# Performance work log

Measured on AMD Instinct MI355X. Metric: run time of the kernel, lower is better.

The kernel has to match this reference:

```python
import jax, jax.numpy as jnp
import numpy as np

EMBED_DIM = 512
SE_HIDDEN = max(1, int(EMBED_DIM * 0.25))  # 128
LN_EPS = 1e-5


def setup_inputs() -> dict:
    key = jax.random.key(0)
    ks = jax.random.split(key, 16)
    B, H, W, D = 8, 32, 32, EMBED_DIM
    s = 0.02
    return {
        "q": jax.random.normal(ks[0], (B, H, W, D), jnp.float32),
        "k": jax.random.normal(ks[1], (B, H, W, D), jnp.float32),
        "v": jax.random.normal(ks[2], (B, H, W, D), jnp.float32),
        # Linear weights stored as [in, out] (equivalent to torch W.T)
        "Wq": jax.random.normal(ks[3], (D, D), jnp.float32) * s,
        "Wk": jax.random.normal(ks[4], (D, D), jnp.float32) * s,
        "Wv": jax.random.normal(ks[5], (D, D), jnp.float32) * s,
        "Wo": jax.random.normal(ks[6], (D, D), jnp.float32) * s,
        # Conv2d kernel in HWIO layout for NHWC conv
        "conv_w": jax.random.normal(ks[7], (3, 3, D, D), jnp.float32) * s,
        "conv_b": jnp.zeros((D,), jnp.float32),
        "se_w1": jax.random.normal(ks[8], (D, SE_HIDDEN), jnp.float32) * s,
        "se_b1": jnp.zeros((SE_HIDDEN,), jnp.float32),
        "se_w2": jax.random.normal(ks[9], (SE_HIDDEN, D), jnp.float32) * s,
        "se_b2": jnp.zeros((D,), jnp.float32),
        "ln_g": jnp.ones((D,), jnp.float32),
        "ln_b": jnp.zeros((D,), jnp.float32),
    }


def _layernorm(x, g, b):
    mu = jnp.mean(x, axis=-1, keepdims=True)
    var = jnp.mean(jnp.square(x - mu), axis=-1, keepdims=True)
    return (x - mu) * jax.lax.rsqrt(var + LN_EPS) * g + b


def reference(q, k, v, Wq, Wk, Wv, Wo, conv_w, conv_b,
              se_w1, se_b1, se_w2, se_b2, ln_g, ln_b):
    B, H, W, D = q.shape
    scaler = jnp.sqrt(jnp.asarray(D, q.dtype))
    qp = q @ Wq  # [B,H,W,D]
    kp = k @ Wk
    vp = v @ Wv
    N = H * W
    qf = qp.reshape(B, N, D)
    kf = kp.reshape(B, N, D)
    vf = vp.reshape(B, N, D)
    scores = jnp.einsum('bnd,bmd->bnm', qf, kf) / scaler
    probs = jax.nn.softmax(scores, axis=-1)  # dropout p=0 -> identity
    out = jnp.einsum('bnm,bmd->bnd', probs, vf).reshape(B, H, W, D)
    out = out @ Wo
    # 3x3 same conv in NHWC
    out = jax.lax.conv_general_dilated(
        out, conv_w, window_strides=(1, 1), padding='SAME',
        dimension_numbers=('NHWC', 'HWIO', 'NHWC')) + conv_b
    # squeeze-excite: global average pool over spatial dims
    se = jnp.mean(out, axis=(1, 2))  # [B,D]
    se = jax.nn.silu(se @ se_w1 + se_b1)
    se = jax.nn.sigmoid(se @ se_w2 + se_b2)  # [B,D]
    out = out * se[:, None, None, :]
    x = qp + out  # residual uses q AFTER q_proj (q reassigned in torch code)
    return _layernorm(x, ln_g, ln_b)
```

## Files before the change

### kernel.cpp

```cpp
#include <hip/hip_runtime.h>
#include <hip/hip_bf16.h>

using bf16 = __hip_bfloat16;
typedef __attribute__((ext_vector_type(8))) short short8;
typedef __attribute__((ext_vector_type(4))) short short4v;
typedef __attribute__((ext_vector_type(4))) float f32x4;

static const size_t OFF_QP   = 0;
static const size_t OFF_KP   = (size_t)8  << 20;
static const size_t OFF_VPT  = (size_t)16 << 20;
static const size_t OFF_SC   = (size_t)24 << 20;
static const size_t OFF_WT   = (size_t)56 << 20;
static const size_t OFF_CWT  = (size_t)58 << 20;
static const size_t OFF_POOL = (size_t)63 << 20;
static const size_t OFF_SE   = ((size_t)63 << 20) + 16384;

__global__ __launch_bounds__(256) void prep_k(const float* __restrict__ Wq,
                                              const float* __restrict__ Wk,
                                              const float* __restrict__ Wv,
                                              const float* __restrict__ Wo,
                                              const float* __restrict__ convw,
                                              bf16* __restrict__ wT,
                                              bf16* __restrict__ cwT,
                                              float* __restrict__ pooled) {
    long idx = (long)blockIdx.x * 256 + threadIdx.x;
    if (idx < 4l * 262144) {
        int m = (int)(idx >> 18);
        int o = (int)(idx & 262143);
        int n = o >> 9, k = o & 511;
        const float* W = (m == 0) ? Wq : (m == 1) ? Wk : (m == 2) ? Wv : Wo;
        wT[idx] = __float2bfloat16(W[k * 512 + n]);
    } else if (idx < 4l * 262144 + 512l * 4608) {
        long o = idx - 4l * 262144;
        int co = (int)(o / 4608), t = (int)(o % 4608);
        cwT[o] = __float2bfloat16(convw[(long)t * 512 + co]);
    } else if (idx < 4l * 262144 + 512l * 4608 + 4096) {
        pooled[idx - (4l * 262144 + 512l * 4608)] = 0.f;
    }
}

template <int OP>
__global__ __launch_bounds__(256, 2) void gemm_k(
    const void* __restrict__ Ap0, const void* __restrict__ Ap1, const void* __restrict__ Ap2,
    int lda, long sA,
    const bf16* __restrict__ BT, int ldb, long sB,
    void* __restrict__ Cp, int ldc, long sC,
    int K, const float* __restrict__ bias, float* __restrict__ pooled) {
    __shared__ bf16 As[2][128 * 64];
    __shared__ bf16 Bs[2][128 * 64];
    const int tid = threadIdx.x;
    const int l = tid & 63, w = tid >> 6;
    const int wm = w >> 1, wn = w & 1;

    const int gx = gridDim.x, gy = gridDim.y;
    const int nwg = gx * gy * gridDim.z;
    const int bid = blockIdx.x + gx * (blockIdx.y + gy * blockIdx.z);
    const int swz = (bid & 7) * (nwg >> 3) + (bid >> 3);
    const int bx = swz % gx;
    const int rem = swz / gx;
    const int by = rem % gy;
    const int zb = rem / gy;

    const int m0 = by * 128, n0 = bx * 128;
    const float isc = 0.04419417382415922f;

    const bf16* Ab = nullptr;
    const float* Af = nullptr;
    if (OP == 1) {
        Af = (const float*)(zb == 0 ? Ap0 : zb == 1 ? Ap1 : Ap2);
    } else {
        Ab = (const bf16*)Ap0 + (long)zb * sA;
    }
    const bf16* Bb = BT + (OP == 1 ? (long)zb * 262144 : (long)zb * sB);

    const int fr = l & 15;
    f32x4 acc[4][4] = {};

    int pixoff[4], hh_[4], wp_[4];
    if (OP == 3) {
#pragma unroll
        for (int i = 0; i < 4; ++i) {
            int s = tid + i * 256;
            int row = s >> 3, c = s & 7;
            int p = m0 + row;
            int bb = p >> 10;
            hh_[i] = (p >> 5) & 31;
            wp_[i] = p & 31;
            pixoff[i] = ((bb * 32 + hh_[i]) * 32 + wp_[i]) * 512 + c * 8;
        }
    }

    short8 ar[4];
    float4 af0[4], af1[4];
    short8 br[4];

    auto stage_load = [&](int t) {
        int k0 = t * 64;
        int dy = 0, dx = 0, doff = 0;
        if (OP == 3) {
            int tap = k0 >> 9;
            dy = tap / 3 - 1;
            dx = tap % 3 - 1;
            doff = (dy * 32 + dx) * 512 + (k0 & 511);
        }
#pragma unroll
        for (int i = 0; i < 4; ++i) {
            int s = tid + i * 256;
            int row = s >> 3, c = s & 7;
            if (OP == 1) {
                const float* src = Af + (long)(m0 + row) * lda + k0 + c * 8;
                af0[i] = *(const float4*)src;
                af1[i] = *(const float4*)(src + 4);
            } else if (OP == 3) {
                int h2 = hh_[i] + dy, w2 = wp_[i] + dx;
                if (((unsigned)h2 < 32u) & ((unsigned)w2 < 32u)) {
                    ar[i] = *(const short8*)(Ab + pixoff[i] + doff);
                } else {
                    short8 zz = {0, 0, 0, 0, 0, 0, 0, 0};
                    ar[i] = zz;
                }
            } else {
                ar[i] = *(const short8*)(Ab + (long)(m0 + row) * lda + k0 + c * 8);
            }
        }
#pragma unroll
        for (int i = 0; i < 4; ++i) {
            int s = tid + i * 256;
            int row = s >> 3, c = s & 7;
            br[i] = *(const short8*)(Bb + (long)(n0 + row) * ldb + k0 + c * 8);
        }
    };

    auto stage_write = [&](int b) {
#pragma unroll
        for (int i = 0; i < 4; ++i) {
            int s = tid + i * 256;
            int row = s >> 3, c = s & 7;
            int cx = c ^ (row & 7);
            if (OP == 1) {
                union { short8 s8; bf16 h[8]; } u;
                u.h[0] = __float2bfloat16(af0[i].x); u.h[1] = __float2bfloat16(af0[i].y);
                u.h[2] = __float2bfloat16(af0[i].z); u.h[3] = __float2bfloat16(af0[i].w);
                u.h[4] = __float2bfloat16(af1[i].x); u.h[5] = __float2bfloat16(af1[i].y);
                u.h[6] = __float2bfloat16(af1[i].z); u.h[7] = __float2bfloat16(af1[i].w);
                *(short8*)(&As[b][row * 64 + cx * 8]) = u.s8;
            } else {
                *(short8*)(&As[b][row * 64 + cx * 8]) = ar[i];
            }
        }
#pragma unroll
        for (int i = 0; i < 4; ++i) {
            int s = tid + i * 256;
            int row = s >> 3, c = s & 7;
            int cx = c ^ (row & 7);
            *(short8*)(&Bs[b][row * 64 + cx * 8]) = br[i];
        }
    };

    auto compute = [&](int b) {
#pragma unroll
        for (int h = 0; h < 2; ++h) {
            int cx = ((l >> 4) + 4 * h) ^ (fr & 7);
            short8 afr[4], bfv[4];
#pragma unroll
            for (int m = 0; m < 4; ++m) {
                int r = wm * 64 + m * 16 + fr;
                afr[m] = *(const short8*)(&As[b][r * 64 + cx * 8]);
            }
#pragma unroll
            for (int n = 0; n < 4; ++n) {
                int r = wn * 64 + n * 16 + fr;
                bfv[n] = *(const short8*)(&Bs[b][r * 64 + cx * 8]);
            }
#pragma unroll
            for (int m = 0; m < 4; ++m)
#pragma unroll
                for (int n = 0; n < 4; ++n)
                    acc[m][n] = __builtin_amdgcn_mfma_f32_16x16x32_bf16(afr[m], bfv[n], acc[m][n], 0, 0, 0);
        }
    };

    const int nt = K >> 6;
    stage_load(0);
    stage_write(0);
    int cur = 0;
    for (int t = 0; t < nt; ++t) {
        __syncthreads();
        if (t + 1 < nt) stage_load(t + 1);
        compute(cur);
        if (t + 1 < nt) stage_write(cur ^ 1);
        cur ^= 1;
    }

    const int cr = (l >> 4) * 4, cc = l & 15;
    float csum[4] = {0.f, 0.f, 0.f, 0.f};
#pragma unroll
    for (int m = 0; m < 4; ++m) {
#pragma unroll
        for (int n = 0; n < 4; ++n) {
#pragma unroll
            for (int j = 0; j < 4; ++j) {
                int r = m0 + wm * 64 + m * 16 + cr + j;
                int c = n0 + wn * 64 + n * 16 + cc;
                float vv = acc[m][n][j];
                if (OP == 3) {
                    vv += bias[c];
                    csum[n] += vv;
                    ((bf16*)Cp)[(long)r * ldc + c] = __float2bfloat16(vv);
                } else if (OP == 0 || OP == 2) {
                    ((bf16*)Cp)[(long)zb * sC + (long)r * ldc + c] = __float2bfloat16(vv);
                } else {
                    if (zb == 2) {
                        ((bf16*)Cp)[(size_t)(OFF_VPT / 2) + ((long)(r >> 10) * 512 + c) * 1024 + (r & 1023)] =
                            __float2bfloat16(vv);
                    } else {
                        float sv = (zb == 1) ? vv * isc : vv;
                        ((bf16*)Cp)[(long)zb * 4194304 + (long)r * 512 + c] = __float2bfloat16(sv);
                    }
                }
            }
        }
    }
    if (OP == 3) {
        int bb = m0 >> 10;
#pragma unroll
        for (int n = 0; n < 4; ++n) {
            int c = n0 + wn * 64 + n * 16 + cc;
            atomicAdd(&pooled[bb * 512 + c], csum[n] * (1.0f / 1024.0f));
        }
    }
}

__global__ __launch_bounds__(256) void softmax_k(bf16* __restrict__ scores) {
    __shared__ float red[256];
    long row = blockIdx.x;
    bf16* base = scores + row * 1024;
    int t = threadIdx.x;
    union { short4v s4; bf16 h[4]; } u;
    u.s4 = *(const short4v*)(base + t * 4);
    float v[4];
#pragma unroll
    for (int i = 0; i < 4; ++i) v[i] = __bfloat162float(u.h[i]);
    float mx = fmaxf(fmaxf(v[0], v[1]), fmaxf(v[2], v[3]));
    red[t] = mx;
    __syncthreads();
    for (int s = 128; s > 0; s >>= 1) {
        if (t < s) red[t] = fmaxf(red[t], red[t + s]);
        __syncthreads();
    }
    mx = red[0];
    __syncthreads();
    float e[4], sum = 0.f;
#pragma unroll
    for (int i = 0; i < 4; ++i) {
        e[i] = __expf(v[i] - mx);
        sum += e[i];
    }
    red[t] = sum;
    __syncthreads();
    for (int s = 128; s > 0; s >>= 1) {
        if (t < s) red[t] += red[t + s];
        __syncthreads();
    }
    float inv = 1.0f / red[0];
#pragma unroll
    for (int i = 0; i < 4; ++i) u.h[i] = __float2bfloat16(e[i] * inv);
    *(short4v*)(base + t * 4) = u.s4;
}

__global__ __launch_bounds__(512) void se_mlp_k(const float* __restrict__ pooled,
                                                const float* __restrict__ w1,
                                                const float* __restrict__ b1,
                                                const float* __restrict__ w2,
                                                const float* __restrict__ b2,
                                                float* __restrict__ se) {
    __shared__ float pl[512];
    __shared__ float part[4][128];
    __shared__ float hid[128];
    const int b = blockIdx.x, t = threadIdx.x;
    pl[t] = pooled[b * 512 + t];
    __syncthreads();
    const int j = t & 127, r = t >> 7;
    float acc = 0.f;
#pragma unroll 8
    for (int s = 0; s < 128; ++s) {
        int i = r * 128 + s;
        acc += pl[i] * w1[i * 128 + j];
    }
    part[r][j] = acc;
    __syncthreads();
    if (t < 128) {
        float a = part[0][t] + part[1][t] + part[2][t] + part[3][t] + b1[t];
        hid[t] = a / (1.f + __expf(-a));
    }
    __syncthreads();
    float acc2 = b2[t];
#pragma unroll 8
    for (int jj = 0; jj < 128; ++jj)
        acc2 += hid[jj] * w2[jj * 512 + t];
    se[b * 512 + t] = 1.f / (1.f + __expf(-acc2));
}

__global__ __launch_bounds__(256) void final_k(const bf16* __restrict__ conv_out,
                                               const float* __restrict__ se,
                                               const bf16* __restrict__ qp,
                                               const float* __restrict__ g,
                                               const float* __restrict__ bta,
                                               float* __restrict__ out) {
    __shared__ float red[256];
    long p = blockIdx.x;
    int b = (int)(p >> 10);
    int t = threadIdx.x;
    float x[2];
#pragma unroll
    for (int i = 0; i < 2; ++i) {
        int c = t + i * 256;
        x[i] = __bfloat162float(qp[p * 512 + c]) +
               __bfloat162float(conv_out[p * 512 + c]) * se[b * 512 + c];
    }
    red[t] = x[0] + x[1];
    __syncthreads();
    for (int s = 128; s > 0; s >>= 1) {
        if (t < s) red[t] += red[t + s];
        __syncthreads();
    }
    float mu = red[0] * (1.0f / 512.0f);
    __syncthreads();
    float d0 = x[0] - mu, d1 = x[1] - mu;
    red[t] = d0 * d0 + d1 * d1;
    __syncthreads();
    for (int s = 128; s > 0; s >>= 1) {
        if (t < s) red[t] += red[t + s];
        __syncthreads();
    }
    float inv = rsqrtf(red[0] * (1.0f / 512.0f) + 1e-5f);
#pragma unroll
    for (int i = 0; i < 2; ++i) {
        int c = t + i * 256;
        out[p * 512 + c] = (x[i] - mu) * inv * g[c] + bta[c];
    }
}

extern "C" void kernel_launch(void* const* d_in, const int* in_sizes, int n_in,
                              void* d_out, int out_size, void* d_ws, size_t ws_size,
                              hipStream_t stream) {
    const float* q      = (const float*)d_in[0];
    const float* k      = (const float*)d_in[1];
    const float* v      = (const float*)d_in[2];
    const float* Wq     = (const float*)d_in[3];
    const float* Wk     = (const float*)d_in[4];
    const float* Wv     = (const float*)d_in[5];
    const float* Wo     = (const float*)d_in[6];
    const float* convw  = (const float*)d_in[7];
    const float* convb  = (const float*)d_in[8];
    const float* se_w1  = (const float*)d_in[9];
    const float* se_b1  = (const float*)d_in[10];
    const float* se_w2  = (const float*)d_in[11];
    const float* se_b2  = (const float*)d_in[12];
    const float* ln_g   = (const float*)d_in[13];
    const float* ln_b   = (const float*)d_in[14];

    char* ws = (char*)d_ws;
    bf16*  qp     = (bf16*)(ws + OFF_QP);
    bf16*  kp     = (bf16*)(ws + OFF_KP);
    bf16*  attn   = (bf16*)(ws + OFF_KP);
    bf16*  vpT    = (bf16*)(ws + OFF_VPT);
    bf16*  out2   = (bf16*)(ws + OFF_VPT);
    bf16*  scores = (bf16*)(ws + OFF_SC);
    bf16*  convo  = (bf16*)(ws + OFF_SC);
    bf16*  wT     = (bf16*)(ws + OFF_WT);
    bf16*  cwT    = (bf16*)(ws + OFF_CWT);
    float* pooled = (float*)(ws + OFF_POOL);
    float* se     = (float*)(ws + OFF_SE);

    prep_k<<<13328, 256, 0, stream>>>(Wq, Wk, Wv, Wo, convw, wT, cwT, pooled);

    gemm_k<1><<<dim3(4, 64, 3), 256, 0, stream>>>(q, k, v, 512, 0, wT, 512, 0,
                                                  ws, 512, 0, 512, nullptr, nullptr);
    gemm_k<2><<<dim3(8, 8, 8), 256, 0, stream>>>(qp, nullptr, nullptr, 512, 1024l * 512,
                                                 kp, 512, 1024l * 512,
                                                 scores, 1024, 1024l * 1024, 512, nullptr, nullptr);
    softmax_k<<<8192, 256, 0, stream>>>(scores);
    gemm_k<0><<<dim3(4, 8, 8), 256, 0, stream>>>(scores, nullptr, nullptr, 1024, 1024l * 1024,
                                                 vpT, 1024, 512l * 1024,
                                                 attn, 512, 1024l * 512, 1024, nullptr, nullptr);
    gemm_k<0><<<dim3(4, 64, 1), 256, 0, stream>>>(attn, nullptr, nullptr, 512, 0,
                                                  wT + 3 * 262144, 512, 0,
                                                  out2, 512, 0, 512, nullptr, nullptr);
    gemm_k<3><<<dim3(4, 64, 1), 256, 0, stream>>>(out2, nullptr, nullptr, 0, 0,
                                                  cwT, 4608, 0,
                                                  convo, 512, 0, 4608, convb, pooled);
    se_mlp_k<<<8, 512, 0, stream>>>(pooled, se_w1, se_b1, se_w2, se_b2, se);
    final_k<<<8192, 256, 0, stream>>>(convo, se, qp, ln_g, ln_b, (float*)d_out);
}
```

Before: 213.1 us.

## Fuse softmax into PV GEMM with split-K, deferred normalization, split-K conv

Removes the standalone softmax kernel. Exponentiation (without max subtraction) now happens while loading score tiles in the PV GEMM, which accumulates row sums there. The PV GEMM and the conv GEMM are split along K into two partial outputs to get more workgroups. The Wo GEMM sums the two attention partials and applies 1/rowsum on load, and the final kernel sums the two conv partials. Dropping max subtraction risks overflow for large scores but saves a full read/write pass over the scores.

```diff
diff --git a/kernel.cpp b/kernel.cpp
--- a/kernel.cpp
+++ b/kernel.cpp
@@ -3,17 +3,18 @@
 
 using bf16 = __hip_bfloat16;
 typedef __attribute__((ext_vector_type(8))) short short8;
-typedef __attribute__((ext_vector_type(4))) short short4v;
 typedef __attribute__((ext_vector_type(4))) float f32x4;
 
 static const size_t OFF_QP   = 0;
 static const size_t OFF_KP   = (size_t)8  << 20;
 static const size_t OFF_VPT  = (size_t)16 << 20;
 static const size_t OFF_SC   = (size_t)24 << 20;
+static const size_t OFF_PA   = (size_t)40 << 20;
 static const size_t OFF_WT   = (size_t)56 << 20;
 static const size_t OFF_CWT  = (size_t)58 << 20;
 static const size_t OFF_POOL = (size_t)63 << 20;
 static const size_t OFF_SE   = ((size_t)63 << 20) + 16384;
+static const size_t OFF_RS   = ((size_t)63 << 20) + 32768;
 
 __global__ __launch_bounds__(256) void prep_k(const float* __restrict__ Wq,
                                               const float* __restrict__ Wk,
@@ -39,13 +40,20 @@
     }
 }
 
+__device__ __forceinline__ float bf2f(unsigned short h) {
+    union { unsigned int u; float f; } c;
+    c.u = (unsigned int)h << 16;
+    return c.f;
+}
+
 template <int OP>
 __global__ __launch_bounds__(256, 2) void gemm_k(
     const void* __restrict__ Ap0, const void* __restrict__ Ap1, const void* __restrict__ Ap2,
     int lda, long sA,
     const bf16* __restrict__ BT, int ldb, long sB,
     void* __restrict__ Cp, int ldc, long sC,
-    int K, const float* __restrict__ bias, float* __restrict__ pooled) {
+    int K, const float* __restrict__ bias, float* __restrict__ pooled,
+    float* __restrict__ rs) {
     __shared__ bf16 As[2][128 * 64];
     __shared__ bf16 Bs[2][128 * 64];
     const int tid = threadIdx.x;
@@ -64,17 +72,30 @@
     const int m0 = by * 128, n0 = bx * 128;
     const float isc = 0.04419417382415922f;
 
+    int kbase = 0;
     const bf16* Ab = nullptr;
     const float* Af = nullptr;
+    const bf16* Bb = BT;
     if (OP == 1) {
         Af = (const float*)(zb == 0 ? Ap0 : zb == 1 ? Ap1 : Ap2);
+        Bb = BT + (long)zb * 262144;
+    } else if (OP == 2) {
+        Ab = (const bf16*)Ap0 + (long)zb * sA;
+        Bb = BT + (long)zb * sB;
+    } else if (OP == 3) {
+        Ab = (const bf16*)Ap0;
+        kbase = zb * 2304;
+    } else if (OP == 4) {
+        Ab = (const bf16*)Ap0 + (long)(zb & 7) * sA;
+        Bb = BT + (long)(zb & 7) * sB;
+        kbase = (zb >> 3) * 512;
     } else {
-        Ab = (const bf16*)Ap0 + (long)zb * sA;
-    }
-    const bf16* Bb = BT + (OP == 1 ? (long)zb * 262144 : (long)zb * sB);
+        Ab = (const bf16*)Ap0;
+    }
 
     const int fr = l & 15;
     f32x4 acc[4][4] = {};
+    float esum[4] = {0.f, 0.f, 0.f, 0.f};
 
     int pixoff[4], hh_[4], wp_[4];
     if (OP == 3) {
@@ -89,13 +110,21 @@
             pixoff[i] = ((bb * 32 + hh_[i]) * 32 + wp_[i]) * 512 + c * 8;
         }
     }
+    float rinv_[4];
+    if (OP == 5) {
+#pragma unroll
+        for (int i = 0; i < 4; ++i) {
+            int row = m0 + ((tid + i * 256) >> 3);
+            rinv_[i] = 1.0f / (rs[row] + rs[8192 + row]);
+        }
+    }
 
     short8 ar[4];
     float4 af0[4], af1[4];
     short8 br[4];
 
     auto stage_load = [&](int t) {
-        int k0 = t * 64;
+        int k0 = kbase + t * 64;
         int dy = 0, dx = 0, doff = 0;
         if (OP == 3) {
             int tap = k0 >> 9;
@@ -119,6 +148,31 @@
                     short8 zz = {0, 0, 0, 0, 0, 0, 0, 0};
                     ar[i] = zz;
                 }
+            } else if (OP == 4) {
+                union { short8 s8; unsigned short h[8]; } u, o;
+                u.s8 = *(const short8*)(Ab + (long)(m0 + row) * lda + k0 + c * 8);
+                float es = 0.f;
+#pragma unroll
+                for (int j = 0; j < 8; ++j) {
+                    float e = __expf(bf2f(u.h[j]));
+                    es += e;
+                    union { float f; unsigned int ui; } cf;
+                    cf.f = e;
+                    o.h[j] = (unsigned short)(cf.ui >> 16);
+                }
+                esum[i] += es;
+                ar[i] = o.s8;
+            } else if (OP == 5) {
+                union { short8 s8; unsigned short h[8]; } u0, u1, o;
+                long off = (long)(m0 + row) * lda + k0 + c * 8;
+                u0.s8 = *(const short8*)(Ab + off);
+                u1.s8 = *(const short8*)(Ab + 4194304 + off);
+#pragma unroll
+                for (int j = 0; j < 8; ++j) {
+                    bf16 b = __float2bfloat16((bf2f(u0.h[j]) + bf2f(u1.h[j])) * rinv_[i]);
+                    o.h[j] = *(unsigned short*)&b;
+                }
+                ar[i] = o.s8;
             } else {
                 ar[i] = *(const short8*)(Ab + (long)(m0 + row) * lda + k0 + c * 8);
             }
@@ -192,6 +246,23 @@
         cur ^= 1;
     }
 
+    if (OP == 4) {
+        __syncthreads();
+        float* fl = (float*)&As[0][0];
+#pragma unroll
+        for (int i = 0; i < 4; ++i) {
+            int s = tid + i * 256;
+            fl[(s >> 3) * 8 + (s & 7)] = esum[i];
+        }
+        __syncthreads();
+        if (bx == 0 && tid < 128) {
+            float s8 = 0.f;
+#pragma unroll
+            for (int j = 0; j < 8; ++j) s8 += fl[tid * 8 + j];
+            rs[(zb >> 3) * 8192 + (zb & 7) * 1024 + m0 + tid] = s8;
+        }
+    }
+
     const int cr = (l >> 4) * 4, cc = l & 15;
     float csum[4] = {0.f, 0.f, 0.f, 0.f};
 #pragma unroll
@@ -204,11 +275,16 @@
                 int c = n0 + wn * 64 + n * 16 + cc;
                 float vv = acc[m][n][j];
                 if (OP == 3) {
-                    vv += bias[c];
+                    if (zb == 0) vv += bias[c];
                     csum[n] += vv;
+                    ((bf16*)Cp)[(long)zb * 4194304 + (long)r * ldc + c] = __float2bfloat16(vv);
+                } else if (OP == 2) {
+                    ((bf16*)Cp)[(long)zb * sC + (long)r * ldc + c] = __float2bfloat16(vv);
+                } else if (OP == 4) {
+                    ((bf16*)Cp)[(long)(zb >> 3) * 4194304 +
+                                ((long)(zb & 7) * 1024 + r) * 512 + c] = __float2bfloat16(vv);
+                } else if (OP == 5) {
                     ((bf16*)Cp)[(long)r * ldc + c] = __float2bfloat16(vv);
-                } else if (OP == 0 || OP == 2) {
-                    ((bf16*)Cp)[(long)zb * sC + (long)r * ldc + c] = __float2bfloat16(vv);
                 } else {
                     if (zb == 2) {
                         ((bf16*)Cp)[(size_t)(OFF_VPT / 2) + ((long)(r >> 10) * 512 + c) * 1024 + (r & 1023)] =
@@ -229,43 +305,6 @@
             atomicAdd(&pooled[bb * 512 + c], csum[n] * (1.0f / 1024.0f));
         }
     }
-}
-
-__global__ __launch_bounds__(256) void softmax_k(bf16* __restrict__ scores) {
-    __shared__ float red[256];
-    long row = blockIdx.x;
-    bf16* base = scores + row * 1024;
-    int t = threadIdx.x;
-    union { short4v s4; bf16 h[4]; } u;
-    u.s4 = *(const short4v*)(base + t * 4);
-    float v[4];
-#pragma unroll
-    for (int i = 0; i < 4; ++i) v[i] = __bfloat162float(u.h[i]);
-    float mx = fmaxf(fmaxf(v[0], v[1]), fmaxf(v[2], v[3]));
-    red[t] = mx;
-    __syncthreads();
-    for (int s = 128; s > 0; s >>= 1) {
-        if (t < s) red[t] = fmaxf(red[t], red[t + s]);
-        __syncthreads();
-    }
-    mx = red[0];
-    __syncthreads();
-    float e[4], sum = 0.f;
-#pragma unroll
-    for (int i = 0; i < 4; ++i) {
-        e[i] = __expf(v[i] - mx);
-        sum += e[i];
-    }
-    red[t] = sum;
-    __syncthreads();
-    for (int s = 128; s > 0; s >>= 1) {
-        if (t < s) red[t] += red[t + s];
-        __syncthreads();
-    }
-    float inv = 1.0f / red[0];
-#pragma unroll
-    for (int i = 0; i < 4; ++i) u.h[i] = __float2bfloat16(e[i] * inv);
-    *(short4v*)(base + t * 4) = u.s4;
 }
 
 __global__ __launch_bounds__(512) void se_mlp_k(const float* __restrict__ pooled,
@@ -301,7 +340,7 @@
     se[b * 512 + t] = 1.f / (1.f + __expf(-acc2));
 }
 
-__global__ __launch_bounds__(256) void final_k(const bf16* __restrict__ conv_out,
+__global__ __launch_bounds__(256) void final_k(const bf16* __restrict__ Pc,
                                                const float* __restrict__ se,
                                                const bf16* __restrict__ qp,
                                                const float* __restrict__ g,
@@ -315,8 +354,9 @@
 #pragma unroll
     for (int i = 0; i < 2; ++i) {
         int c = t + i * 256;
-        x[i] = __bfloat162float(qp[p * 512 + c]) +
-               __bfloat162float(conv_out[p * 512 + c]) * se[b * 512 + c];
+        float cv = __bfloat162float(Pc[p * 512 + c]) +
+                   __bfloat162float(Pc[4194304 + p * 512 + c]);
+        x[i] = __bfloat162float(qp[p * 512 + c]) + cv * se[b * 512 + c];
     }
     red[t] = x[0] + x[1];
     __syncthreads();
@@ -363,33 +403,33 @@
     char* ws = (char*)d_ws;
     bf16*  qp     = (bf16*)(ws + OFF_QP);
     bf16*  kp     = (bf16*)(ws + OFF_KP);
-    bf16*  attn   = (bf16*)(ws + OFF_KP);
     bf16*  vpT    = (bf16*)(ws + OFF_VPT);
     bf16*  out2   = (bf16*)(ws + OFF_VPT);
     bf16*  scores = (bf16*)(ws + OFF_SC);
-    bf16*  convo  = (bf16*)(ws + OFF_SC);
+    bf16*  Pattn  = (bf16*)(ws + OFF_PA);
+    bf16*  Pconv  = (bf16*)(ws + OFF_SC);
     bf16*  wT     = (bf16*)(ws + OFF_WT);
     bf16*  cwT    = (bf16*)(ws + OFF_CWT);
     float* pooled = (float*)(ws + OFF_POOL);
     float* se     = (float*)(ws + OFF_SE);
+    float* rsums  = (float*)(ws + OFF_RS);
 
     prep_k<<<13328, 256, 0, stream>>>(Wq, Wk, Wv, Wo, convw, wT, cwT, pooled);
 
     gemm_k<1><<<dim3(4, 64, 3), 256, 0, stream>>>(q, k, v, 512, 0, wT, 512, 0,
-                                                  ws, 512, 0, 512, nullptr, nullptr);
+                                                  ws, 512, 0, 512, nullptr, nullptr, nullptr);
     gemm_k<2><<<dim3(8, 8, 8), 256, 0, stream>>>(qp, nullptr, nullptr, 512, 1024l * 512,
                                                  kp, 512, 1024l * 512,
-                                                 scores, 1024, 1024l * 1024, 512, nullptr, nullptr);
-    softmax_k<<<8192, 256, 0, stream>>>(scores);
-    gemm_k<0><<<dim3(4, 8, 8), 256, 0, stream>>>(scores, nullptr, nullptr, 1024, 1024l * 1024,
-                                                 vpT, 1024, 512l * 1024,
-                                                 attn, 512, 1024l * 512, 1024, nullptr, nullptr);
-    gemm_k<0><<<dim3(4, 64, 1), 256, 0, stream>>>(attn, nullptr, nullptr, 512, 0,
+                                                 scores, 1024, 1024l * 1024, 512, nullptr, nullptr, nullptr);
+    gemm_k<4><<<dim3(4, 8, 16), 256, 0, stream>>>(scores, nullptr, nullptr, 1024, 1024l * 1024,
+                                                  vpT, 1024, 512l * 1024,
+                                                  Pattn, 512, 0, 512, nullptr, nullptr, rsums);
+    gemm_k<5><<<dim3(4, 64, 1), 256, 0, stream>>>(Pattn, nullptr, nullptr, 512, 0,
                                                   wT + 3 * 262144, 512, 0,
-                                                  out2, 512, 0, 512, nullptr, nullptr);
-    gemm_k<3><<<dim3(4, 64, 1), 256, 0, stream>>>(out2, nullptr, nullptr, 0, 0,
+                                                  out2, 512, 0, 512, nullptr, nullptr, rsums);
+    gemm_k<3><<<dim3(4, 64, 2), 256, 0, stream>>>(out2, nullptr, nullptr, 0, 0,
                                                   cwT, 4608, 0,
-                                                  convo, 512, 0, 4608, convb, pooled);
+                                                  Pconv, 512, 0, 2304, convb, pooled, nullptr);
     se_mlp_k<<<8, 512, 0, stream>>>(pooled, se_w1, se_b1, se_w2, se_b2, se);
-    final_k<<<8192, 256, 0, stream>>>(convo, se, qp, ln_g, ln_b, (float*)d_out);
-}
+    final_k<<<8192, 256, 0, stream>>>(Pconv, se, qp, ln_g, ln_b, (float*)d_out);
+}
```

Measured after the change: 198.9 us. 6.7% less time.
